# Optimization experiments

Hardware: AMD Instinct MI355X
Metric: run time of the kernel (lower is better)

Reference implementation:

```python
import jax, jax.numpy as jnp
import numpy as np
import math

B, T, C = 8, 2048, 1024
KEY_SIZE, VALUE_SIZE = 1024, 1024


def setup_inputs() -> dict:
    key = jax.random.key(0)
    ks = jax.random.split(key, 7)
    s = 1.0 / math.sqrt(C)
    return {
        "input": jax.random.normal(ks[0], (B, T, C), dtype=jnp.float32),
        "mask": jnp.ones((B, T, 1), dtype=jnp.float32),
        "Wq": jax.random.uniform(ks[1], (C, KEY_SIZE), jnp.float32, -s, s),
        "bq": jax.random.uniform(ks[2], (KEY_SIZE,), jnp.float32, -s, s),
        "Wk": jax.random.uniform(ks[3], (C, KEY_SIZE), jnp.float32, -s, s),
        "bk": jax.random.uniform(ks[4], (KEY_SIZE,), jnp.float32, -s, s),
        "Wv": jax.random.uniform(ks[5], (C, VALUE_SIZE), jnp.float32, -s, s),
        "bv": jax.random.uniform(ks[6], (VALUE_SIZE,), jnp.float32, -s, s),
    }


def reference(input, mask, Wq, bq, Wk, bk, Wv, bv):
    # QKV projections: [B, T, C] @ [C, K] -> [B, T, K]
    query = input @ Wq + bq
    keys = input @ Wk + bk
    values = input @ Wv + bv
    # scores[b, tq, tk] = query[b, tq, :] . keys[b, tk, :]
    scores = jnp.einsum("bqk,btk->bqt", query, keys) / math.sqrt(KEY_SIZE)
    # NOTE: softmax over the QUERY dimension (axis=1), as in the original (dim=1)
    attn = jax.nn.softmax(scores, axis=1)
    out = jnp.einsum("bqt,btv->bqv", attn, values)
    return out * mask
```

## Files before the change

### kernel.cpp

```cpp
#include <hip/hip_runtime.h>
#include <hip/hip_bf16.h>
#include <cstdint>

typedef __attribute__((ext_vector_type(8))) __bf16 bf16x8;
typedef __attribute__((ext_vector_type(4))) float f32x4;
typedef __attribute__((ext_vector_type(8))) unsigned short u16x8;

static __device__ __forceinline__ unsigned short f2b(float f) {
    union { float f; unsigned u; } v; v.f = f;
    unsigned r = v.u + 0x7fffu + ((v.u >> 16) & 1u);
    return (unsigned short)(r >> 16);
}
static __device__ __forceinline__ float b2f(unsigned short b) {
    union { unsigned u; float f; } v; v.u = ((unsigned)b) << 16;
    return v.f;
}

#define LL16(g, l) __builtin_amdgcn_global_load_lds( \
    (const __attribute__((address_space(1))) void*)(g), \
    (__attribute__((address_space(3))) void*)(l), 16, 0, 0)

#define BAR() __builtin_amdgcn_s_barrier()
#define WAIT_VM8() asm volatile("s_waitcnt vmcnt(8)" ::: "memory")
#define WAIT_VM0() asm volatile("s_waitcnt vmcnt(0)" ::: "memory")

__global__ void conv_f32_bf16(const float* __restrict__ in,
                              unsigned short* __restrict__ out, long n8) {
    long i = (long)blockIdx.x * blockDim.x + threadIdx.x;
    if (i >= n8) return;
    const float4* p = (const float4*)in + i * 2;
    float4 a = p[0], b = p[1];
    u16x8 r;
    r[0] = f2b(a.x); r[1] = f2b(a.y); r[2] = f2b(a.z); r[3] = f2b(a.w);
    r[4] = f2b(b.x); r[5] = f2b(b.y); r[6] = f2b(b.z); r[7] = f2b(b.w);
    *(u16x8*)(out + i * 8) = r;
}

__global__ void transpose_w(const float* __restrict__ w0,
                            const float* __restrict__ w1,
                            const float* __restrict__ w2,
                            unsigned short* __restrict__ out) {
    __shared__ float tile[32][33];
    int z = blockIdx.z;
    const float* W = (z == 0) ? w0 : (z == 1) ? w1 : w2;
    int n0 = blockIdx.x * 32, c0 = blockIdx.y * 32;
    int tx = threadIdx.x & 31, ty = threadIdx.x >> 5;
    #pragma unroll
    for (int i = 0; i < 32; i += 8)
        tile[ty + i][tx] = W[(long)(c0 + ty + i) * 1024 + n0 + tx];
    __syncthreads();
    unsigned short* o = out + (long)z * 1024 * 1024;
    #pragma unroll
    for (int i = 0; i < 32; i += 8)
        o[(long)(n0 + ty + i) * 1024 + c0 + tx] = f2b(tile[tx][ty + i]);
}

__global__ void scale_vt(unsigned short* __restrict__ Vt,
                         const float* __restrict__ colsum) {
    long i8 = ((long)blockIdx.x * 256 + threadIdx.x) * 8;
    int b = (int)(i8 >> 21);
    int rem = (int)(i8 & ((1 << 21) - 1));
    int t = rem & 2047;
    const float* cs = colsum + b * 2048 + t;
    u16x8 v = *(const u16x8*)(Vt + i8);
    u16x8 o;
    #pragma unroll
    for (int j = 0; j < 8; ++j) o[j] = f2b(b2f(v[j]) / cs[j]);
    *(u16x8*)(Vt + i8) = o;
}


template<int MODE>
__global__ __launch_bounds__(256, 2)
void gemm128(const unsigned short* __restrict__ Aall,
             const unsigned short* __restrict__ Ball,
             void* __restrict__ Cv,
             int M, int N, int K, int ldc,
             long aStride, long bStride, long cStride,
             const float* __restrict__ aux, float* __restrict__ colsum) {
    __shared__ unsigned short lds[32768];

    const int gx = gridDim.x, gy = gridDim.y;
    const int nxy = gx * gy;
    const int nwg = nxy * gridDim.z;
    const int orig = (blockIdx.z * gy + blockIdx.y) * gx + blockIdx.x;
    const int swz = (orig & 7) * (nwg >> 3) + (orig >> 3);
    const int bz = swz / nxy;
    const int rem = swz - bz * nxy;
    const int sb = rem / (gy * 4);
    const int r2 = rem - sb * (gy * 4);
    const int by = r2 >> 2;
    const int bx = sb * 4 + (r2 & 3);

    const unsigned short* A  = Aall + (long)bz * aStride;
    const unsigned short* Bt = Ball + (long)bz * bStride;

    const int tid = threadIdx.x;
    const int lane = tid & 63;
    const int w = tid >> 6;
    const int wrow = w >> 1, wcol = w & 1;
    const int lr = lane & 15, lg = lane >> 4;

    const int bm = by * 128, bn = bx * 128;
    const int NT = K >> 6;

    const int r0 = tid >> 3;
    const int c0 = (tid & 7) ^ (r0 & 7);
    const unsigned short* sA0 = A  + (long)(bm + r0)      * K + c0 * 8;
    const unsigned short* sA1 = A  + (long)(bm + 32 + r0) * K + c0 * 8;
    const unsigned short* sA2 = A  + (long)(bm + 64 + r0) * K + c0 * 8;
    const unsigned short* sA3 = A  + (long)(bm + 96 + r0) * K + c0 * 8;
    const unsigned short* sB0 = Bt + (long)(bn + r0)      * K + c0 * 8;
    const unsigned short* sB1 = Bt + (long)(bn + 32 + r0) * K + c0 * 8;
    const unsigned short* sB2 = Bt + (long)(bn + 64 + r0) * K + c0 * 8;
    const unsigned short* sB3 = Bt + (long)(bn + 96 + r0) * K + c0 * 8;
    const int dstT = tid * 8;

    const int cx0 = (lg ^ (lr & 7)) * 8;
    const int cx1 = ((4 + lg) ^ (lr & 7)) * 8;
    const int baA = (wrow * 64 + lr) * 64;
    const int baB = (wcol * 64 + lr) * 64;

    bf16x8 af[4][2], bf[4][2];
    f32x4 acc[4][4] = {};

    #define STAGE(kt, buf) do { const long ko = (long)(kt) * 64; \
        LL16(sA0 + ko, lds + (buf) * 8192 + dstT); \
        LL16(sA1 + ko, lds + (buf) * 8192 + 2048 + dstT); \
        LL16(sA2 + ko, lds + (buf) * 8192 + 4096 + dstT); \
        LL16(sA3 + ko, lds + (buf) * 8192 + 6144 + dstT); \
        LL16(sB0 + ko, lds + 16384 + (buf) * 8192 + dstT); \
        LL16(sB1 + ko, lds + 16384 + (buf) * 8192 + 2048 + dstT); \
        LL16(sB2 + ko, lds + 16384 + (buf) * 8192 + 4096 + dstT); \
        LL16(sB3 + ko, lds + 16384 + (buf) * 8192 + 6144 + dstT); } while (0)

    STAGE(0, 0);
    STAGE(1, 1);

    for (int t = 0; t < NT; ++t) {
        if (t < NT - 1) { WAIT_VM8(); } else { WAIT_VM0(); }
        BAR();

        const int aB = (t & 1) * 8192;
        const int bB = 16384 + (t & 1) * 8192;
        #pragma unroll
        for (int mi = 0; mi < 4; ++mi) {
            af[mi][0] = *(const bf16x8*)(lds + aB + baA + mi * 1024 + cx0);
            af[mi][1] = *(const bf16x8*)(lds + aB + baA + mi * 1024 + cx1);
        }
        #pragma unroll
        for (int nj = 0; nj < 4; ++nj) {
            bf[nj][0] = *(const bf16x8*)(lds + bB + baB + nj * 1024 + cx0);
            bf[nj][1] = *(const bf16x8*)(lds + bB + baB + nj * 1024 + cx1);
        }
        __builtin_amdgcn_s_setprio(1);
        #pragma unroll
        for (int mi = 0; mi < 4; ++mi)
            #pragma unroll
            for (int nj = 0; nj < 4; ++nj) {
                acc[mi][nj] = __builtin_amdgcn_mfma_f32_16x16x32_bf16(
                    af[mi][0], bf[nj][0], acc[mi][nj], 0, 0, 0);
                acc[mi][nj] = __builtin_amdgcn_mfma_f32_16x16x32_bf16(
                    af[mi][1], bf[nj][1], acc[mi][nj], 0, 0, 0);
            }
        __builtin_amdgcn_s_setprio(0);

        BAR();
        if (t + 2 < NT) STAGE(t + 2, t & 1);
    }
    #undef STAGE

    if (MODE != 3) {
        unsigned short* C = (unsigned short*)Cv + (long)bz * cStride;
        float* cs = colsum + (long)bz * 2048;
        #pragma unroll
        for (int nj = 0; nj < 4; ++nj) {
            const int cl = wcol * 64 + nj * 16 + lr;
            const int cb = cl >> 3, cIn = cl & 7;
            float colB = (MODE == 0) ? aux[bn + cl] : 0.f;
            float psum = 0.f;
            #pragma unroll
            for (int mi = 0; mi < 4; ++mi) {
                #pragma unroll
                for (int r = 0; r < 4; ++r) {
                    const int rl = wrow * 64 + mi * 16 + lg * 4 + r;
                    float v = acc[mi][nj][r];
                    if (MODE == 0) v += colB;
                    else if (MODE == 1) v += aux[bm + rl];
                    else { v = __expf(v * 0.03125f); psum += v; }
                    lds[rl * 128 + ((cb ^ ((rl & 7) << 1)) << 3) + cIn] = f2b(v);
                }
            }
            if (MODE == 2) {
                psum += __shfl_xor(psum, 16);
                psum += __shfl_xor(psum, 32);
                if (lg == 0) atomicAdd(&cs[bn + cl], psum);
            }
        }
        BAR();
        #pragma unroll
        for (int it = 0; it < 8; ++it) {
            int lin = it * 256 + tid;
            int row = lin >> 4;
            int c = lin & 15;
            u16x8 v = *(const u16x8*)&lds[row * 128 + ((c ^ ((row & 7) << 1)) << 3)];
            *(u16x8*)&C[(long)(bm + row) * ldc + bn + c * 8] = v;
        }
    } else {
        float* C = (float*)Cv + (long)bz * cStride;
        const float* mk = aux + (long)bz * 2048;
        float* ft = (float*)lds;
        #pragma unroll
        for (int nj = 0; nj < 4; ++nj) {
            const int cl = wcol * 64 + nj * 16 + lr;
            const int cf = cl >> 2, cIn = cl & 3;
            #pragma unroll
            for (int mi = 0; mi < 4; ++mi) {
                #pragma unroll
                for (int r = 0; r < 4; ++r) {
                    const int rl = wrow * 64 + mi * 16 + lg * 4 + r;
                    ft[rl * 128 + ((cf ^ ((rl & 7) << 2)) << 2) + cIn] =
                        acc[mi][nj][r] * mk[bm + rl];
                }
            }
        }
        BAR();
        #pragma unroll
        for (int it = 0; it < 16; ++it) {
            int lin = it * 256 + tid;
            int row = lin >> 5;
            int cf = lin & 31;
            float4 v = *(const float4*)&ft[row * 128 + ((cf ^ ((row & 7) << 2)) << 2)];
            *(float4*)&C[(long)(bm + row) * ldc + bn + cf * 4] = v;
        }
    }
}

extern "C" void kernel_launch(void* const* d_in, const int* in_sizes, int n_in,
                              void* d_out, int out_size, void* d_ws, size_t ws_size,
                              hipStream_t stream) {
    const float* x    = (const float*)d_in[0];
    const float* mask = (const float*)d_in[1];
    const float* Wq   = (const float*)d_in[2];
    const float* bq   = (const float*)d_in[3];
    const float* Wk   = (const float*)d_in[4];
    const float* bk   = (const float*)d_in[5];
    const float* Wv   = (const float*)d_in[6];
    const float* bv   = (const float*)d_in[7];
    float* out = (float*)d_out;

    const long MT = 16384;
    unsigned short* Xb = (unsigned short*)d_ws;
    unsigned short* Wt = Xb + MT * 1024;
    unsigned short* Q  = Wt + 3L * 1024 * 1024;
    unsigned short* Kk = Q  + MT * 1024;
    unsigned short* Vt = Kk + MT * 1024;
    unsigned short* E  = Vt + 8L * 1024 * 2048;
    float* colsum = (float*)(E + 8L * 2048 * 2048);
    size_t need = (size_t)((char*)(colsum + 8 * 2048) - (char*)d_ws);
    if (ws_size < need) return;

    conv_f32_bf16<<<(MT * 1024) / 8 / 256, 256, 0, stream>>>(x, Xb, (MT * 1024) / 8);
    transpose_w<<<dim3(32, 32, 3), 256, 0, stream>>>(Wq, Wk, Wv, Wt);
    gemm128<0><<<dim3(8, 128, 1), 256, 0, stream>>>(
        Xb, Wt, Q, 16384, 1024, 1024, 1024, 0, 0, 0, bq, nullptr);
    gemm128<0><<<dim3(8, 128, 1), 256, 0, stream>>>(
        Xb, Wt + 1048576, Kk, 16384, 1024, 1024, 1024, 0, 0, 0, bk, nullptr);
    gemm128<1><<<dim3(16, 8, 8), 256, 0, stream>>>(
        Wt + 2097152, Xb, Vt, 1024, 2048, 1024, 2048,
        0, 2048L * 1024, 1024L * 2048, bv, nullptr);
    hipMemsetAsync(colsum, 0, 8 * 2048 * sizeof(float), stream);
    gemm128<2><<<dim3(16, 16, 8), 256, 0, stream>>>(
        Q, Kk, E, 2048, 2048, 1024, 2048,
        2048L * 1024, 2048L * 1024, 2048L * 2048, nullptr, colsum);
    scale_vt<<<8192, 256, 0, stream>>>(Vt, colsum);
    gemm128<3><<<dim3(8, 16, 8), 256, 0, stream>>>(
        E, Vt, out, 2048, 1024, 2048, 1024,
        2048L * 2048, 1024L * 2048, 2048L * 1024, mask, nullptr);
}
```

Baseline: 311.8 us.

## Fold Wq·Wkᵀ into one weight matrix, replacing Q and K projections

The attention scores are rewritten as X·(Wq·Wkᵀ)·Xᵀ plus rank-one bias terms. A small 1024x1024 GEMM forms Z = Wq·Wkᵀ, one large GEMM computes Y = X·Z, and the score GEMM uses Y against X directly. The bias cross terms (X·Wq·bk, X·Wk·bq, bq·bk) are computed as per-row vectors during the input conversion and added in the exp epilogue. This removes one full 16384x1024x1024 projection GEMM. In exchange it adds atomics in the conversion kernel and rounds Z to bf16, which changes numerical error.

```diff
diff --git a/kernel.cpp b/kernel.cpp
--- a/kernel.cpp
+++ b/kernel.cpp
@@ -36,23 +36,86 @@
     *(u16x8*)(out + i * 8) = r;
 }
 
-__global__ void transpose_w(const float* __restrict__ w0,
-                            const float* __restrict__ w1,
-                            const float* __restrict__ w2,
-                            unsigned short* __restrict__ out) {
+__global__ void conv_x(const float* __restrict__ in,
+                       unsigned short* __restrict__ out,
+                       const float* __restrict__ wqbk,
+                       const float* __restrict__ wkbq,
+                       float* __restrict__ u, float* __restrict__ v) {
+    long i = (long)blockIdx.x * blockDim.x + threadIdx.x;
+    const float4* p = (const float4*)in + i * 2;
+    float4 a = p[0], b = p[1];
+    u16x8 r;
+    r[0] = f2b(a.x); r[1] = f2b(a.y); r[2] = f2b(a.z); r[3] = f2b(a.w);
+    r[4] = f2b(b.x); r[5] = f2b(b.y); r[6] = f2b(b.z); r[7] = f2b(b.w);
+    *(u16x8*)(out + i * 8) = r;
+    const int c = (int)(i & 127) * 8;
+    const long row = i >> 7;
+    const float* wq = wqbk + c;
+    const float* wk = wkbq + c;
+    float du = a.x*wq[0] + a.y*wq[1] + a.z*wq[2] + a.w*wq[3]
+             + b.x*wq[4] + b.y*wq[5] + b.z*wq[6] + b.w*wq[7];
+    float dv = a.x*wk[0] + a.y*wk[1] + a.z*wk[2] + a.w*wk[3]
+             + b.x*wk[4] + b.y*wk[5] + b.z*wk[6] + b.w*wk[7];
+    #pragma unroll
+    for (int s = 1; s < 64; s <<= 1) {
+        du += __shfl_xor(du, s);
+        dv += __shfl_xor(dv, s);
+    }
+    if ((threadIdx.x & 63) == 0) {
+        atomicAdd(&u[row], du);
+        atomicAdd(&v[row], dv);
+    }
+}
+
+__global__ void wdots(const float* __restrict__ Wq, const float* __restrict__ bq,
+                      const float* __restrict__ Wk, const float* __restrict__ bk,
+                      float* __restrict__ wqbk, float* __restrict__ wkbq,
+                      float* __restrict__ cbuf) {
+    const int lane = threadIdx.x & 63;
+    if (blockIdx.x == 256) {
+        float s = 0.f;
+        for (int k = threadIdx.x; k < 1024; k += 256) s += bq[k] * bk[k];
+        #pragma unroll
+        for (int sh = 1; sh < 64; sh <<= 1) s += __shfl_xor(s, sh);
+        __shared__ float ps[4];
+        if (lane == 0) ps[threadIdx.x >> 6] = s;
+        __syncthreads();
+        if (threadIdx.x == 0) cbuf[0] = ps[0] + ps[1] + ps[2] + ps[3];
+        return;
+    }
+    const int c = blockIdx.x * 4 + (threadIdx.x >> 6);
+    const float* wq = Wq + (long)c * 1024;
+    const float* wk = Wk + (long)c * 1024;
+    float sq = 0.f, sk = 0.f;
+    for (int k0 = 0; k0 < 1024; k0 += 256) {
+        int k = k0 + lane * 4;
+        float4 q4 = *(const float4*)(wq + k);
+        float4 k4 = *(const float4*)(wk + k);
+        float4 b4 = *(const float4*)(bk + k);
+        float4 a4 = *(const float4*)(bq + k);
+        sq += q4.x*b4.x + q4.y*b4.y + q4.z*b4.z + q4.w*b4.w;
+        sk += k4.x*a4.x + k4.y*a4.y + k4.z*a4.z + k4.w*a4.w;
+    }
+    #pragma unroll
+    for (int sh = 1; sh < 64; sh <<= 1) {
+        sq += __shfl_xor(sq, sh);
+        sk += __shfl_xor(sk, sh);
+    }
+    if (lane == 0) { wqbk[c] = sq; wkbq[c] = sk; }
+}
+
+__global__ void transpose_wv(const float* __restrict__ W,
+                             unsigned short* __restrict__ out) {
     __shared__ float tile[32][33];
-    int z = blockIdx.z;
-    const float* W = (z == 0) ? w0 : (z == 1) ? w1 : w2;
     int n0 = blockIdx.x * 32, c0 = blockIdx.y * 32;
     int tx = threadIdx.x & 31, ty = threadIdx.x >> 5;
     #pragma unroll
     for (int i = 0; i < 32; i += 8)
         tile[ty + i][tx] = W[(long)(c0 + ty + i) * 1024 + n0 + tx];
     __syncthreads();
-    unsigned short* o = out + (long)z * 1024 * 1024;
     #pragma unroll
     for (int i = 0; i < 32; i += 8)
-        o[(long)(n0 + ty + i) * 1024 + c0 + tx] = f2b(tile[tx][ty + i]);
+        out[(long)(n0 + ty + i) * 1024 + c0 + tx] = f2b(tile[tx][ty + i]);
 }
 
 __global__ void scale_vt(unsigned short* __restrict__ Vt,
@@ -173,22 +236,25 @@
     if (MODE != 3) {
         unsigned short* C = (unsigned short*)Cv + (long)bz * cStride;
         float* cs = colsum + (long)bz * 2048;
+        const float cQK = (MODE == 2) ? aux[32768] : 0.f;
         #pragma unroll
         for (int nj = 0; nj < 4; ++nj) {
             const int cl = wcol * 64 + nj * 16 + lr;
             const int cb = cl >> 3, cIn = cl & 7;
-            float colB = (MODE == 0) ? aux[bn + cl] : 0.f;
+            float vcol = (MODE == 2) ? (aux[16384 + bz * 2048 + bn + cl] + cQK) : 0.f;
             float psum = 0.f;
             #pragma unroll
             for (int mi = 0; mi < 4; ++mi) {
                 #pragma unroll
                 for (int r = 0; r < 4; ++r) {
                     const int rl = wrow * 64 + mi * 16 + lg * 4 + r;
-                    float v = acc[mi][nj][r];
-                    if (MODE == 0) v += colB;
-                    else if (MODE == 1) v += aux[bm + rl];
-                    else { v = __expf(v * 0.03125f); psum += v; }
-                    lds[rl * 128 + ((cb ^ ((rl & 7) << 1)) << 3) + cIn] = f2b(v);
+                    float val = acc[mi][nj][r];
+                    if (MODE == 1) val += aux[bm + rl];
+                    else if (MODE == 2) {
+                        val = __expf((val + aux[bz * 2048 + bm + rl] + vcol) * 0.03125f);
+                        psum += val;
+                    }
+                    lds[rl * 128 + ((cb ^ ((rl & 7) << 1)) << 3) + cIn] = f2b(val);
                 }
             }
             if (MODE == 2) {
@@ -250,29 +316,39 @@
     float* out = (float*)d_out;
 
     const long MT = 16384;
-    unsigned short* Xb = (unsigned short*)d_ws;
-    unsigned short* Wt = Xb + MT * 1024;
-    unsigned short* Q  = Wt + 3L * 1024 * 1024;
-    unsigned short* Kk = Q  + MT * 1024;
-    unsigned short* Vt = Kk + MT * 1024;
-    unsigned short* E  = Vt + 8L * 1024 * 2048;
+    unsigned short* Xb  = (unsigned short*)d_ws;
+    unsigned short* Wqb = Xb + MT * 1024;
+    unsigned short* Wkb = Wqb + 1048576;
+    unsigned short* Wvt = Wkb + 1048576;
+    unsigned short* Y   = Wvt + 1048576;
+    unsigned short* Z   = Y + MT * 1024;
+    unsigned short* Vt  = Z + MT * 1024;
+    unsigned short* E   = Vt + 8L * 1024 * 2048;
     float* colsum = (float*)(E + 8L * 2048 * 2048);
-    size_t need = (size_t)((char*)(colsum + 8 * 2048) - (char*)d_ws);
+    float* u      = colsum + 16384;
+    float* v      = u + 16384;
+    float* cbuf   = v + 16384;
+    float* wqbk   = cbuf + 1;
+    float* wkbq   = wqbk + 1024;
+    size_t need = (size_t)((char*)(wkbq + 1024) - (char*)d_ws);
     if (ws_size < need) return;
 
-    conv_f32_bf16<<<(MT * 1024) / 8 / 256, 256, 0, stream>>>(x, Xb, (MT * 1024) / 8);
-    transpose_w<<<dim3(32, 32, 3), 256, 0, stream>>>(Wq, Wk, Wv, Wt);
+    hipMemsetAsync(colsum, 0, 3L * 16384 * sizeof(float), stream);
+    wdots<<<257, 256, 0, stream>>>(Wq, bq, Wk, bk, wqbk, wkbq, cbuf);
+    conv_x<<<8192, 256, 0, stream>>>(x, Xb, wqbk, wkbq, u, v);
+    conv_f32_bf16<<<512, 256, 0, stream>>>(Wq, Wqb, 131072);
+    conv_f32_bf16<<<512, 256, 0, stream>>>(Wk, Wkb, 131072);
+    transpose_wv<<<dim3(32, 32), 256, 0, stream>>>(Wv, Wvt);
+    gemm128<0><<<dim3(8, 8, 1), 256, 0, stream>>>(
+        Wkb, Wqb, Z, 1024, 1024, 1024, 1024, 0, 0, 0, nullptr, nullptr);
     gemm128<0><<<dim3(8, 128, 1), 256, 0, stream>>>(
-        Xb, Wt, Q, 16384, 1024, 1024, 1024, 0, 0, 0, bq, nullptr);
-    gemm128<0><<<dim3(8, 128, 1), 256, 0, stream>>>(
-        Xb, Wt + 1048576, Kk, 16384, 1024, 1024, 1024, 0, 0, 0, bk, nullptr);
+        Xb, Z, Y, 16384, 1024, 1024, 1024, 0, 0, 0, nullptr, nullptr);
     gemm128<1><<<dim3(16, 8, 8), 256, 0, stream>>>(
-        Wt + 2097152, Xb, Vt, 1024, 2048, 1024, 2048,
+        Wvt, Xb, Vt, 1024, 2048, 1024, 2048,
         0, 2048L * 1024, 1024L * 2048, bv, nullptr);
-    hipMemsetAsync(colsum, 0, 8 * 2048 * sizeof(float), stream);
     gemm128<2><<<dim3(16, 16, 8), 256, 0, stream>>>(
-        Q, Kk, E, 2048, 2048, 1024, 2048,
-        2048L * 1024, 2048L * 1024, 2048L * 2048, nullptr, colsum);
+        Y, Xb, E, 2048, 2048, 1024, 2048,
+        2048L * 1024, 2048L * 1024, 2048L * 2048, u, colsum);
     scale_vt<<<8192, 256, 0, stream>>>(Vt, colsum);
     gemm128<3><<<dim3(8, 16, 8), 256, 0, stream>>>(
         E, Vt, out, 2048, 1024, 2048, 1024,
```

Measured after the change: 298.9 us. 1.04x faster.
